# Kernel tuning notes

Measured on AMD Instinct MI355X. Metric: run time of the kernel, lower is better.

## Reference

```python
import jax, jax.numpy as jnp
import numpy as np

EPS = 1e-12
ALPHA = 0.2  # LeakyReLU negative slope
N_NODES = 100000
N_EDGES = 1600000
F = 128
H = 8

def setup_inputs() -> dict:
    key = jax.random.key(0)
    k1, k2, k3, k4 = jax.random.split(key, 4)
    x = jax.random.normal(k1, (N_NODES, F), dtype=jnp.float32)
    row = jax.random.randint(k2, (N_EDGES,), 0, N_NODES, dtype=jnp.int32)
    col = jax.random.randint(k3, (N_EDGES,), 0, N_NODES, dtype=jnp.int32)
    # xavier_uniform with gain=1.414 on [H, 2F]
    limit = 1.414 * np.sqrt(6.0 / (H + 2 * F))
    aa = jax.random.uniform(k4, (H, 2 * F), dtype=jnp.float32, minval=-limit, maxval=limit)
    return {"x": x, "row": row, "col": col, "aa": aa}

def reference(x, row, col, aa):
    # e = leakyrelu(aa @ cat(x[row], x[col], dim=1).T)  -> [H, E]
    # Split aa so per-node scores are computed once, then gathered per edge
    # (identical math, avoids materializing the [E, 2F] concat).
    a_src, a_dst = aa[:, :F], aa[:, F:]          # [H, F] each
    s_src = x @ a_src.T                           # [N, H]
    s_dst = x @ a_dst.T                           # [N, H]
    e = s_src[row] + s_dst[col]                   # [E, H]
    e = jnp.where(e > 0, e, ALPHA * e)            # LeakyReLU
    # scatter_softmax over edges grouped by row (per head)
    m = jax.ops.segment_max(e, row, num_segments=N_NODES)  # [N, H]
    m = jnp.where(jnp.isfinite(m), m, 0.0)        # empty segments -> -inf; neutralize
    ex = jnp.exp(e - m[row])                      # [E, H]
    s = jax.ops.segment_sum(ex, row, num_segments=N_NODES)  # [N, H]
    a = ex / (s[row] + EPS)                       # [E, H]
    return a.T                                    # [H, E] to match torch layout
```

## Files before the change

### kernel.cpp

```cpp
#include <hip/hip_runtime.h>

constexpr int N_NODES = 100000;
constexpr int N_EDGES = 1600000;
constexpr int F = 128;
constexpr int H = 8;
constexpr float ALPHA = 0.2f;
constexpr float EPSF = 1e-12f;

constexpr int PSHIFT = 8;
constexpr int PN = 1 << PSHIFT;
constexpr int NPART = (N_NODES + PN - 1) / PN;
constexpr int MAXPART = 5120;
constexpr int EPB = 4096;
constexpr int OCAP = 4096;

__global__ void k1_scores(const float* __restrict__ x, const float* __restrict__ aa,
                          float* __restrict__ srn, float* __restrict__ sd) {
    __shared__ float sa[H * 2 * F];
    for (int i = threadIdx.x; i < H * 2 * F; i += blockDim.x) sa[i] = aa[i];
    __syncthreads();
    int node = blockIdx.x * blockDim.x + threadIdx.x;
    if (node >= N_NODES) return;
    const float4* xr = reinterpret_cast<const float4*>(x + (size_t)node * F);
    float accs[H], accd[H];
#pragma unroll
    for (int h = 0; h < H; ++h) { accs[h] = 0.f; accd[h] = 0.f; }
    for (int f4 = 0; f4 < F / 4; ++f4) {
        float4 xv = xr[f4];
#pragma unroll
        for (int h = 0; h < H; ++h) {
            float4 av = *reinterpret_cast<const float4*>(&sa[h * 2 * F + 4 * f4]);
            float4 bv = *reinterpret_cast<const float4*>(&sa[h * 2 * F + F + 4 * f4]);
            accs[h] += xv.x * av.x + xv.y * av.y + xv.z * av.z + xv.w * av.w;
            accd[h] += xv.x * bv.x + xv.y * bv.y + xv.z * bv.z + xv.w * bv.w;
        }
    }
    float4* os = reinterpret_cast<float4*>(srn + (size_t)node * 16);
    os[0] = make_float4(accs[0], accs[1], accs[2], accs[3]);
    os[1] = make_float4(accs[4], accs[5], accs[6], accs[7]);
    float4* od = reinterpret_cast<float4*>(sd + (size_t)node * H);
    od[0] = make_float4(accd[0], accd[1], accd[2], accd[3]);
    od[1] = make_float4(accd[4], accd[5], accd[6], accd[7]);
}

__global__ void __launch_bounds__(1024)
kA_part(const int* __restrict__ row, const int* __restrict__ col,
        int* __restrict__ gcnt, unsigned* __restrict__ part,
        int* __restrict__ ocnt, int2* __restrict__ olist) {
    __shared__ int hist[NPART];
    __shared__ int base[NPART];
    const int t = threadIdx.x;
    const int e0 = blockIdx.x * EPB;
    for (int p = t; p < NPART; p += 1024) hist[p] = 0;
    __syncthreads();
    for (int k = 0; k < EPB / 1024; ++k) {
        int i = e0 + k * 1024 + t;
        if (i < N_EDGES) atomicAdd(&hist[row[i] >> PSHIFT], 1);
    }
    __syncthreads();
    for (int p = t; p < NPART; p += 1024) {
        int h = hist[p];
        base[p] = h ? atomicAdd(&gcnt[p], h) : 0;
        hist[p] = 0;
    }
    __syncthreads();
    for (int k = 0; k < EPB / 1024; ++k) {
        int i = e0 + k * 1024 + t;
        if (i < N_EDGES) {
            int r = row[i], c = col[i];
            int p = r >> PSHIFT;
            int slot = base[p] + atomicAdd(&hist[p], 1);
            unsigned pk = ((unsigned)(r & (PN - 1)) << 17) | (unsigned)c;
            if (slot < MAXPART) {
                part[(size_t)p * MAXPART + slot] = pk;
            } else {
                int q = atomicAdd(ocnt, 1);
                if (q < OCAP) olist[q] = make_int2(p, (int)pk);
            }
        }
    }
}

__global__ void __launch_bounds__(1024)
kB_sum(const float* __restrict__ sd, const unsigned* __restrict__ part,
       const int* __restrict__ gcnt, const int* __restrict__ ocnt,
       const int2* __restrict__ olist, float* __restrict__ srn) {
    __shared__ unsigned plist[MAXPART];
    __shared__ unsigned sorted_c[MAXPART];
    __shared__ int hist[PN];
    __shared__ int off[PN + 1];
    __shared__ int cur[PN];
    __shared__ float ssrc[PN * H];
    const int p = blockIdx.x;
    const int t = threadIdx.x;
    const int nbase = p << PSHIFT;

    for (int i = t; i < PN; i += 1024) hist[i] = 0;
    for (int j = t; j < PN * H; j += 1024) {
        int n = nbase + (j >> 3);
        ssrc[j] = (n < N_NODES) ? srn[(size_t)n * 16 + (j & 7)] : 0.f;
    }
    __syncthreads();

    int cnt = gcnt[p]; if (cnt > MAXPART) cnt = MAXPART;
    const unsigned* pp = part + (size_t)p * MAXPART;

    for (int i = t; i < cnt; i += 1024) {
        unsigned pk = pp[i];
        plist[i] = pk;
        atomicAdd(&hist[pk >> 17], 1);
    }
    __syncthreads();

    for (int d = 1; d < PN; d <<= 1) {
        int add = 0;
        if (t >= d && t < PN) add = hist[t - d];
        __syncthreads();
        if (t < PN) hist[t] += add;
        __syncthreads();
    }
    if (t < PN) off[t + 1] = hist[t];
    if (t == 0) off[0] = 0;
    __syncthreads();
    if (t < PN) cur[t] = off[t];
    __syncthreads();

    for (int i = t; i < cnt; i += 1024) {
        unsigned pk = plist[i];
        int rl = (int)(pk >> 17);
        int slot = atomicAdd(&cur[rl], 1);
        sorted_c[slot] = pk & 0x1FFFFu;
    }
    __syncthreads();

    int mo = *ocnt; if (mo > OCAP) mo = OCAP;
    {
        int nl = t >> 2, pi = t & 3;
        int node = nbase + nl;
        int k0 = off[nl], k1e = off[nl + 1];
        float s0 = ssrc[nl * 8 + 2 * pi];
        float s1 = ssrc[nl * 8 + 2 * pi + 1];
        float a0 = 0.f, a1 = 0.f;
        int k = k0;
        for (; k + 4 <= k1e; k += 4) {
            int c0 = (int)sorted_c[k],     c1 = (int)sorted_c[k + 1];
            int c2 = (int)sorted_c[k + 2], c3 = (int)sorted_c[k + 3];
            float2 d0 = *reinterpret_cast<const float2*>(&sd[(size_t)c0 * H + 2 * pi]);
            float2 d1 = *reinterpret_cast<const float2*>(&sd[(size_t)c1 * H + 2 * pi]);
            float2 d2 = *reinterpret_cast<const float2*>(&sd[(size_t)c2 * H + 2 * pi]);
            float2 d3 = *reinterpret_cast<const float2*>(&sd[(size_t)c3 * H + 2 * pi]);
            float e;
            e = s0 + d0.x; e = e > 0.f ? e : ALPHA * e; a0 += __expf(e);
            e = s1 + d0.y; e = e > 0.f ? e : ALPHA * e; a1 += __expf(e);
            e = s0 + d1.x; e = e > 0.f ? e : ALPHA * e; a0 += __expf(e);
            e = s1 + d1.y; e = e > 0.f ? e : ALPHA * e; a1 += __expf(e);
            e = s0 + d2.x; e = e > 0.f ? e : ALPHA * e; a0 += __expf(e);
            e = s1 + d2.y; e = e > 0.f ? e : ALPHA * e; a1 += __expf(e);
            e = s0 + d3.x; e = e > 0.f ? e : ALPHA * e; a0 += __expf(e);
            e = s1 + d3.y; e = e > 0.f ? e : ALPHA * e; a1 += __expf(e);
        }
        for (; k < k1e; ++k) {
            int c = (int)sorted_c[k];
            float2 d = *reinterpret_cast<const float2*>(&sd[(size_t)c * H + 2 * pi]);
            float e0 = s0 + d.x; e0 = e0 > 0.f ? e0 : ALPHA * e0;
            float e1 = s1 + d.y; e1 = e1 > 0.f ? e1 : ALPHA * e1;
            a0 += __expf(e0); a1 += __expf(e1);
        }
        for (int j = 0; j < mo; ++j) {
            int2 oe = olist[j];
            if (oe.x == p && (int)(((unsigned)oe.y) >> 17) == nl) {
                int c = oe.y & 0x1FFFF;
                float2 d = *reinterpret_cast<const float2*>(&sd[(size_t)c * H + 2 * pi]);
                float e0 = s0 + d.x; e0 = e0 > 0.f ? e0 : ALPHA * e0;
                float e1 = s1 + d.y; e1 = e1 > 0.f ? e1 : ALPHA * e1;
                a0 += __expf(e0); a1 += __expf(e1);
            }
        }
        if (node < N_NODES) {
            srn[(size_t)node * 16 + 8 + 2 * pi]     = 1.f / (a0 + EPSF);
            srn[(size_t)node * 16 + 8 + 2 * pi + 1] = 1.f / (a1 + EPSF);
        }
    }
}

__global__ void __launch_bounds__(256)
k4_out(const int* __restrict__ row, const int* __restrict__ col,
       const float* __restrict__ srn, const float* __restrict__ sd,
       float* __restrict__ out) {
    int i0 = (blockIdx.x * blockDim.x + threadIdx.x) * 2;
    if (i0 >= N_EDGES) return;
    int2 rr = *reinterpret_cast<const int2*>(&row[i0]);
    int2 cc = *reinterpret_cast<const int2*>(&col[i0]);
    const float4* srA = reinterpret_cast<const float4*>(srn + (size_t)rr.x * 16);
    const float4* srB = reinterpret_cast<const float4*>(srn + (size_t)rr.y * 16);
    const float4* scA = reinterpret_cast<const float4*>(sd + (size_t)cc.x * H);
    const float4* scB = reinterpret_cast<const float4*>(sd + (size_t)cc.y * H);
    float4 sA0 = srA[0], sA1 = srA[1], rA0 = srA[2], rA1 = srA[3];
    float4 sB0 = srB[0], sB1 = srB[1], rB0 = srB[2], rB1 = srB[3];
    float4 dA0 = scA[0], dA1 = scA[1];
    float4 dB0 = scB[0], dB1 = scB[1];
    float eA[H] = {sA0.x + dA0.x, sA0.y + dA0.y, sA0.z + dA0.z, sA0.w + dA0.w,
                   sA1.x + dA1.x, sA1.y + dA1.y, sA1.z + dA1.z, sA1.w + dA1.w};
    float eB[H] = {sB0.x + dB0.x, sB0.y + dB0.y, sB0.z + dB0.z, sB0.w + dB0.w,
                   sB1.x + dB1.x, sB1.y + dB1.y, sB1.z + dB1.z, sB1.w + dB1.w};
    float vA[H] = {rA0.x, rA0.y, rA0.z, rA0.w, rA1.x, rA1.y, rA1.z, rA1.w};
    float vB[H] = {rB0.x, rB0.y, rB0.z, rB0.w, rB1.x, rB1.y, rB1.z, rB1.w};
#pragma unroll
    for (int h = 0; h < H; ++h) {
        float a = eA[h] > 0.f ? eA[h] : ALPHA * eA[h];
        float b = eB[h] > 0.f ? eB[h] : ALPHA * eB[h];
        float2 o = make_float2(__expf(a) * vA[h], __expf(b) * vB[h]);
        *reinterpret_cast<float2*>(&out[(size_t)h * N_EDGES + i0]) = o;
    }
}

__global__ void kz_zero_sums(float* __restrict__ srn) {
    int t = blockIdx.x * blockDim.x + threadIdx.x;
    if (t >= N_NODES * H) return;
    srn[(size_t)(t >> 3) * 16 + 8 + (t & 7)] = 0.f;
}

__global__ void k3nm_sum(const float* __restrict__ srn_ro, const float* __restrict__ s_dst,
                         const int* __restrict__ row, const int* __restrict__ col,
                         float* __restrict__ srn) {
    int i = blockIdx.x * blockDim.x + threadIdx.x;
    if (i >= N_EDGES) return;
    int r = row[i], c = col[i];
    const float4* sr = reinterpret_cast<const float4*>(srn_ro + (size_t)r * 16);
    float4 a0 = sr[0], a1 = sr[1];
    const float4* sc = reinterpret_cast<const float4*>(s_dst + (size_t)c * H);
    float4 b0 = sc[0], b1 = sc[1];
    float ev[H] = {a0.x + b0.x, a0.y + b0.y, a0.z + b0.z, a0.w + b0.w,
                   a1.x + b1.x, a1.y + b1.y, a1.z + b1.z, a1.w + b1.w};
#pragma unroll
    for (int h = 0; h < H; ++h) {
        float e = ev[h] > 0.f ? ev[h] : ALPHA * ev[h];
        atomicAdd(&srn[(size_t)r * 16 + 8 + h], __expf(e));
    }
}

__global__ void k_inv(float* __restrict__ srn) {
    int t = blockIdx.x * blockDim.x + threadIdx.x;
    if (t >= N_NODES * H) return;
    int n = t >> 3, h = t & 7;
    float s = srn[(size_t)n * 16 + 8 + h];
    srn[(size_t)n * 16 + 8 + h] = 1.0f / (s + EPSF);
}

extern "C" void kernel_launch(void* const* d_in, const int* in_sizes, int n_in,
                              void* d_out, int out_size, void* d_ws, size_t ws_size,
                              hipStream_t stream) {
    const float* x   = (const float*)d_in[0];
    const int*   row = (const int*)d_in[1];
    const int*   col = (const int*)d_in[2];
    const float* aa  = (const float*)d_in[3];
    float* out = (float*)d_out;

    float*    srn  = (float*)d_ws;
    float*    sd   = srn + (size_t)N_NODES * 16;
    unsigned* part = (unsigned*)(sd + (size_t)N_NODES * H);
    int*      gcnt = (int*)(part + (size_t)NPART * MAXPART);
    int*      ocnt = gcnt + NPART;
    int2*     olist = (int2*)(ocnt + 16);

    const size_t need_b = ((size_t)N_NODES * 24 + (size_t)NPART * MAXPART
                           + NPART + 16 + 2 * OCAP) * 4;

    const int B = 256;
    const int GE  = (N_EDGES + B - 1) / B;
    const int GE2 = (N_EDGES + 2 * B - 1) / (2 * B);
    const int GN  = (N_NODES + B - 1) / B;

    k1_scores<<<GN, B, 0, stream>>>(x, aa, srn, sd);

    if (ws_size >= need_b) {
        hipMemsetAsync(gcnt, 0, (size_t)(NPART + 16) * sizeof(int), stream);
        kA_part<<<(N_EDGES + EPB - 1) / EPB, 1024, 0, stream>>>(row, col, gcnt, part, ocnt, olist);
        kB_sum<<<NPART, 1024, 0, stream>>>(sd, part, gcnt, ocnt, olist, srn);
    } else {
        kz_zero_sums<<<(N_NODES * H + B - 1) / B, B, 0, stream>>>(srn);
        k3nm_sum<<<GE, B, 0, stream>>>(srn, sd, row, col, srn);
        k_inv<<<(N_NODES * H + B - 1) / B, B, 0, stream>>>(srn);
    }

    k4_out<<<GE2, B, 0, stream>>>(row, col, srn, sd, out);
}
```

Before: 214.7 us.

## Use shared-memory transpose for edge output and cache row/col in registers

Replaces the per-edge output kernel with one that gives each thread one (edge, head) pair. The thread gathers its scalar score terms, stages results in shared memory, and writes each head's 64 outputs as contiguous coalesced stores. The partition kernel now keeps row/col values in registers between its histogram and scatter passes instead of reloading them from global memory. The fallback path keeps a simpler one-edge-per-thread output kernel. The trade is more scalar gathers and two barriers per block in exchange for better write coalescing.

```diff
diff --git a/kernel.cpp b/kernel.cpp
--- a/kernel.cpp
+++ b/kernel.cpp
@@ -13,6 +13,8 @@
 constexpr int MAXPART = 5120;
 constexpr int EPB = 4096;
 constexpr int OCAP = 4096;
+
+static_assert(N_EDGES % 64 == 0, "k4_hs assumes 64-edge blocks");
 
 __global__ void k1_scores(const float* __restrict__ x, const float* __restrict__ aa,
                           float* __restrict__ srn, float* __restrict__ sd) {
@@ -51,11 +53,18 @@
     __shared__ int base[NPART];
     const int t = threadIdx.x;
     const int e0 = blockIdx.x * EPB;
+    constexpr int K = EPB / 1024;
+    int rr[K], cc[K];
     for (int p = t; p < NPART; p += 1024) hist[p] = 0;
     __syncthreads();
-    for (int k = 0; k < EPB / 1024; ++k) {
+#pragma unroll
+    for (int k = 0; k < K; ++k) {
         int i = e0 + k * 1024 + t;
-        if (i < N_EDGES) atomicAdd(&hist[row[i] >> PSHIFT], 1);
+        if (i < N_EDGES) {
+            rr[k] = row[i];
+            cc[k] = col[i];
+            atomicAdd(&hist[rr[k] >> PSHIFT], 1);
+        } else rr[k] = -1;
     }
     __syncthreads();
     for (int p = t; p < NPART; p += 1024) {
@@ -64,10 +73,10 @@
         hist[p] = 0;
     }
     __syncthreads();
-    for (int k = 0; k < EPB / 1024; ++k) {
-        int i = e0 + k * 1024 + t;
-        if (i < N_EDGES) {
-            int r = row[i], c = col[i];
+#pragma unroll
+    for (int k = 0; k < K; ++k) {
+        if (rr[k] >= 0) {
+            int r = rr[k], c = cc[k];
             int p = r >> PSHIFT;
             int slot = base[p] + atomicAdd(&hist[p], 1);
             unsigned pk = ((unsigned)(r & (PN - 1)) << 17) | (unsigned)c;
@@ -183,34 +192,31 @@
     }
 }
 
-__global__ void __launch_bounds__(256)
-k4_out(const int* __restrict__ row, const int* __restrict__ col,
-       const float* __restrict__ srn, const float* __restrict__ sd,
-       float* __restrict__ out) {
-    int i0 = (blockIdx.x * blockDim.x + threadIdx.x) * 2;
-    if (i0 >= N_EDGES) return;
-    int2 rr = *reinterpret_cast<const int2*>(&row[i0]);
-    int2 cc = *reinterpret_cast<const int2*>(&col[i0]);
-    const float4* srA = reinterpret_cast<const float4*>(srn + (size_t)rr.x * 16);
-    const float4* srB = reinterpret_cast<const float4*>(srn + (size_t)rr.y * 16);
-    const float4* scA = reinterpret_cast<const float4*>(sd + (size_t)cc.x * H);
-    const float4* scB = reinterpret_cast<const float4*>(sd + (size_t)cc.y * H);
-    float4 sA0 = srA[0], sA1 = srA[1], rA0 = srA[2], rA1 = srA[3];
-    float4 sB0 = srB[0], sB1 = srB[1], rB0 = srB[2], rB1 = srB[3];
-    float4 dA0 = scA[0], dA1 = scA[1];
-    float4 dB0 = scB[0], dB1 = scB[1];
-    float eA[H] = {sA0.x + dA0.x, sA0.y + dA0.y, sA0.z + dA0.z, sA0.w + dA0.w,
-                   sA1.x + dA1.x, sA1.y + dA1.y, sA1.z + dA1.z, sA1.w + dA1.w};
-    float eB[H] = {sB0.x + dB0.x, sB0.y + dB0.y, sB0.z + dB0.z, sB0.w + dB0.w,
-                   sB1.x + dB1.x, sB1.y + dB1.y, sB1.z + dB1.z, sB1.w + dB1.w};
-    float vA[H] = {rA0.x, rA0.y, rA0.z, rA0.w, rA1.x, rA1.y, rA1.z, rA1.w};
-    float vB[H] = {rB0.x, rB0.y, rB0.z, rB0.w, rB1.x, rB1.y, rB1.z, rB1.w};
-#pragma unroll
-    for (int h = 0; h < H; ++h) {
-        float a = eA[h] > 0.f ? eA[h] : ALPHA * eA[h];
-        float b = eB[h] > 0.f ? eB[h] : ALPHA * eB[h];
-        float2 o = make_float2(__expf(a) * vA[h], __expf(b) * vB[h]);
-        *reinterpret_cast<float2*>(&out[(size_t)h * N_EDGES + i0]) = o;
+__global__ void __launch_bounds__(512)
+k4_hs(const int* __restrict__ row, const int* __restrict__ col,
+      const float* __restrict__ srn, const float* __restrict__ sd,
+      float* __restrict__ out) {
+    __shared__ int ridx[64], cidx[64];
+    __shared__ float sm[8][72];
+    const int e0 = blockIdx.x * 64;
+    const int t = threadIdx.x;
+    if (t < 64) ridx[t] = row[e0 + t];
+    else if (t < 128) cidx[t - 64] = col[e0 + t - 64];
+    __syncthreads();
+    {
+        int el = t >> 3, h = t & 7;
+        int r = ridx[el], c = cidx[el];
+        float s  = srn[(size_t)r * 16 + h];
+        float rv = srn[(size_t)r * 16 + 8 + h];
+        float d  = sd[(size_t)c * H + h];
+        float e = s + d;
+        e = e > 0.f ? e : ALPHA * e;
+        sm[h][el] = __expf(e) * rv;
+    }
+    __syncthreads();
+    {
+        int h2 = t >> 6, j = t & 63;
+        out[(size_t)h2 * N_EDGES + e0 + j] = sm[h2][j];
     }
 }
 
@@ -247,6 +253,26 @@
     srn[(size_t)n * 16 + 8 + h] = 1.0f / (s + EPSF);
 }
 
+__global__ void k4_out(const int* __restrict__ row, const int* __restrict__ col,
+                       const float* __restrict__ srn, const float* __restrict__ s_dst,
+                       float* __restrict__ out) {
+    int i = blockIdx.x * blockDim.x + threadIdx.x;
+    if (i >= N_EDGES) return;
+    int r = row[i], c = col[i];
+    const float4* sr = reinterpret_cast<const float4*>(srn + (size_t)r * 16);
+    float4 a0 = sr[0], a1 = sr[1], r0 = sr[2], r1 = sr[3];
+    const float4* sc = reinterpret_cast<const float4*>(s_dst + (size_t)c * H);
+    float4 b0 = sc[0], b1 = sc[1];
+    float ev[H] = {a0.x + b0.x, a0.y + b0.y, a0.z + b0.z, a0.w + b0.w,
+                   a1.x + b1.x, a1.y + b1.y, a1.z + b1.z, a1.w + b1.w};
+    float rv[H] = {r0.x, r0.y, r0.z, r0.w, r1.x, r1.y, r1.z, r1.w};
+#pragma unroll
+    for (int h = 0; h < H; ++h) {
+        float e = ev[h] > 0.f ? ev[h] : ALPHA * ev[h];
+        out[(size_t)h * N_EDGES + i] = __expf(e) * rv[h];
+    }
+}
+
 extern "C" void kernel_launch(void* const* d_in, const int* in_sizes, int n_in,
                               void* d_out, int out_size, void* d_ws, size_t ws_size,
                               hipStream_t stream) {
@@ -268,7 +294,6 @@
 
     const int B = 256;
     const int GE  = (N_EDGES + B - 1) / B;
-    const int GE2 = (N_EDGES + 2 * B - 1) / (2 * B);
     const int GN  = (N_NODES + B - 1) / B;
 
     k1_scores<<<GN, B, 0, stream>>>(x, aa, srn, sd);
@@ -277,11 +302,11 @@
         hipMemsetAsync(gcnt, 0, (size_t)(NPART + 16) * sizeof(int), stream);
         kA_part<<<(N_EDGES + EPB - 1) / EPB, 1024, 0, stream>>>(row, col, gcnt, part, ocnt, olist);
         kB_sum<<<NPART, 1024, 0, stream>>>(sd, part, gcnt, ocnt, olist, srn);
+        k4_hs<<<N_EDGES / 64, 512, 0, stream>>>(row, col, srn, sd, out);
     } else {
         kz_zero_sums<<<(N_NODES * H + B - 1) / B, B, 0, stream>>>(srn);
         k3nm_sum<<<GE, B, 0, stream>>>(srn, sd, row, col, srn);
         k_inv<<<(N_NODES * H + B - 1) / B, B, 0, stream>>>(srn);
-    }
-
-    k4_out<<<GE2, B, 0, stream>>>(row, col, srn, sd, out);
-}
+        k4_out<<<GE, B, 0, stream>>>(row, col, srn, sd, out);
+    }
+}
```

New measurement: 205.8 us. 1.04x faster.
